# Optimization experiments

Hardware: AMD Instinct MI355X
Metric: run time of the kernel (lower is better)

The kernel has to match this reference:

```python
import jax, jax.numpy as jnp
import numpy as np

B, T = 64, 256
IN, HID, OUT = 512, 1024, 256
NUM_DOMAINS = 20

def setup_inputs() -> dict:
    key = jax.random.key(0)
    k1, k2, k3, k4 = jax.random.split(key, 4)
    x = jax.random.normal(k1, (B, T, IN), dtype=jnp.float32)
    hetero_info = jax.random.randint(k2, (B, 2), 0, NUM_DOMAINS, dtype=jnp.int64)
    # embedding tables init N(0, 0.02) as in the torch module
    fc1_table = 0.02 * jax.random.normal(k3, (NUM_DOMAINS, IN * HID + HID), dtype=jnp.float32)
    fc2_table = 0.02 * jax.random.normal(k4, (NUM_DOMAINS, HID * OUT + OUT), dtype=jnp.float32)
    return {"x": x, "hetero_info": hetero_info, "fc1_table": fc1_table, "fc2_table": fc2_table}

def reference(x, hetero_info, fc1_table, fc2_table):
    domain_id = hetero_info[:, 0].astype(jnp.int32)
    Bn = domain_id.shape[0]
    fc1_param = fc1_table[domain_id]                     # (B, IN*HID + HID)
    w1 = fc1_param[:, : IN * HID].reshape(Bn, IN, HID)   # (B, IN, HID)
    b1 = fc1_param[:, IN * HID:].reshape(Bn, 1, HID)
    fc2_param = fc2_table[domain_id]                     # (B, HID*OUT + OUT)
    w2 = fc2_param[:, : HID * OUT].reshape(Bn, HID, OUT) # (B, HID, OUT)
    b2 = fc2_param[:, HID * OUT:].reshape(Bn, 1, OUT)
    h = jnp.einsum('bti,bih->bth', x, w1) + b1
    h = jax.nn.gelu(h, approximate=False)  # torch nn.GELU default = exact erf
    out = jnp.einsum('bth,bho->bto', h, w2) + b2
    return out
```

## Files before the change

### kernel.cpp

```cpp
#include <hip/hip_runtime.h>
#include <math.h>

#define B_  64
#define T_  256
#define IN_ 512
#define HID_ 1024
#define OUT_ 256
#define NDOM 20

typedef __bf16 bf16_t;
typedef __bf16 bf16x8 __attribute__((ext_vector_type(8)));
typedef __bf16 bf16x4 __attribute__((ext_vector_type(4)));
typedef float  f32x4  __attribute__((ext_vector_type(4)));

__device__ __forceinline__ unsigned f2bf_bits(float f) {
    unsigned u = __builtin_bit_cast(unsigned, f);
    return (u + 0x7FFFu + ((u >> 16) & 1u)) >> 16;
}
__device__ __forceinline__ unsigned pack_bf16x2(float x, float y) {
    return f2bf_bits(x) | (f2bf_bits(y) << 16);
}

__device__ __forceinline__ void gl_lds16(const void* g, void* l) {
    __builtin_amdgcn_global_load_lds(
        (const __attribute__((address_space(1))) unsigned*)g,
        (__attribute__((address_space(3))) unsigned*)l,
        16, 0, 0);
}

__device__ __forceinline__ float gelu_fast(float v) {
    const float t = v * 0.70710678118654752f;
    const float a = __builtin_fabsf(t);
    const float k = __builtin_amdgcn_rcpf(__builtin_fmaf(0.3275911f, a, 1.0f));
    float p = __builtin_fmaf(1.061405429f, k, -1.453152027f);
    p = __builtin_fmaf(p, k, 1.421413741f);
    p = __builtin_fmaf(p, k, -0.284496736f);
    p = __builtin_fmaf(p, k, 0.254829592f);
    p = p * k;
    const float e  = __expf(-a * a);
    const float er = __builtin_fmaf(-p, e, 1.0f);
    const float erf_t = __builtin_copysignf(er, t);
    return 0.5f * v * (1.0f + erf_t);
}

template<int K, int N>
__global__ __launch_bounds__(256) void cvt_transpose(
    const float* __restrict__ table, bf16_t* __restrict__ Wt, float* __restrict__ BiasOut)
{
    const int d  = blockIdx.z;
    const float* W = table + (size_t)d * ((size_t)K * N + N);
    const int n0 = blockIdx.x * 64;
    const int k0 = blockIdx.y * 64;
    const int tid = threadIdx.x;

    __shared__ float t[64][65];

    #pragma unroll
    for (int r = 0; r < 4; ++r) {
        const int kl = (tid >> 4) + r * 16;
        const int nl = (tid & 15) * 4;
        float4 v = *(const float4*)(W + (size_t)(k0 + kl) * N + n0 + nl);
        t[kl][nl + 0] = v.x; t[kl][nl + 1] = v.y;
        t[kl][nl + 2] = v.z; t[kl][nl + 3] = v.w;
    }
    __syncthreads();

    bf16_t* Wtd = Wt + (size_t)d * K * N;
    #pragma unroll
    for (int r = 0; r < 4; ++r) {
        const int nl = (tid >> 4) + r * 16;
        const int k4 = (tid & 15) * 4;
        uint2 p;
        p.x = pack_bf16x2(t[k4 + 0][nl], t[k4 + 1][nl]);
        p.y = pack_bf16x2(t[k4 + 2][nl], t[k4 + 3][nl]);
        *(uint2*)(Wtd + (size_t)(n0 + nl) * K + k0 + k4) = p;
    }

    if (blockIdx.y == 0 && tid < 64)
        BiasOut[(size_t)d * N + n0 + tid] = W[(size_t)K * N + n0 + tid];
}

#define CT_STRIDE 136
__global__ __launch_bounds__(256) void fc1_gemm(
    const float*  __restrict__ X,
    const bf16_t* __restrict__ W1t,
    const float*  __restrict__ Bias,
    const int*    __restrict__ hetero,
    bf16_t*       __restrict__ H)
{
    const int id   = blockIdx.x;
    const int g    = id & 127;
    const int nidx = id >> 7;
    const int b    = g >> 1;
    const int m0   = (g & 1) * 128;
    const int n0   = nidx * 128;
    const int d    = hetero[2 * b];
    const bf16_t* W    = W1t + (size_t)d * HID_ * IN_;
    const float*  bias = Bias + (size_t)d * HID_;
    const float*  A    = X + (size_t)(b * 256 + m0) * IN_;

    __shared__ __attribute__((aligned(16))) char smem[65536];

    const int tid  = threadIdx.x;
    const int wave = tid >> 6;
    const int lane = tid & 63;
    const int l16  = lane & 15;
    const int quad = lane >> 4;
    const int wm   = (wave >> 1) * 64;
    const int wn   = (wave & 1) * 64;

    const int arow0 = tid >> 4;
    const int acol4 = tid & 15;

    f32x4 acc[4][4] = {};
    float4 pre[8];

    auto ldsA = [&](int nb) -> bf16_t* { return (bf16_t*)(smem + nb * 16384); };
    auto ldsB = [&](int nb) -> bf16_t* { return (bf16_t*)(smem + 32768 + nb * 16384); };

    auto loadA = [&](int kk) {
        #pragma unroll
        for (int r = 0; r < 8; ++r)
            pre[r] = *(const float4*)(A + (size_t)(arow0 + r * 16) * IN_ + kk + acol4 * 4);
    };
    auto writeA = [&](bf16_t* dst) {
        #pragma unroll
        for (int r = 0; r < 8; ++r) {
            const int row = arow0 + r * 16;
            const int cs  = (acol4 >> 1) ^ (row & 7);
            bf16x4 w;
            w[0] = (bf16_t)pre[r].x; w[1] = (bf16_t)pre[r].y;
            w[2] = (bf16_t)pre[r].z; w[3] = (bf16_t)pre[r].w;
            *(bf16x4*)&dst[row * 64 + cs * 8 + (acol4 & 1) * 4] = w;
        }
    };
    auto stageB = [&](int kk, bf16_t* dst) {
        #pragma unroll
        for (int cc = 0; cc < 4; ++cc) {
            const int r0  = wave * 32 + cc * 8;
            const int row = r0 + (lane >> 3);
            const int cs  = (lane & 7) ^ (row & 7);
            gl_lds16(W + (size_t)(n0 + row) * IN_ + kk + cs * 8, dst + r0 * 64);
        }
    };
    auto compute = [&](const bf16_t* La, const bf16_t* Lb) {
        #pragma unroll
        for (int h = 0; h < 2; ++h) {
            bf16x8 af[4], bfg[4];
            #pragma unroll
            for (int i = 0; i < 4; ++i) {
                const int r = wm + i * 16 + l16;
                const int c = (h * 4 + quad) ^ (r & 7);
                af[i] = *(const bf16x8*)&La[r * 64 + c * 8];
            }
            #pragma unroll
            for (int j = 0; j < 4; ++j) {
                const int r = wn + j * 16 + l16;
                const int c = (h * 4 + quad) ^ (r & 7);
                bfg[j] = *(const bf16x8*)&Lb[r * 64 + c * 8];
            }
            #pragma unroll
            for (int i = 0; i < 4; ++i)
                #pragma unroll
                for (int j = 0; j < 4; ++j)
                    acc[i][j] = __builtin_amdgcn_mfma_f32_16x16x32_bf16(bfg[j], af[i], acc[i][j], 0, 0, 0);
        }
    };

    loadA(0);
    stageB(0, ldsB(0));
    writeA(ldsA(0));
    __syncthreads();

    int buf = 0;
    for (int s = 0; s < 7; ++s) {
        loadA((s + 1) * 64);
        stageB((s + 1) * 64, ldsB(buf ^ 1));
        compute(ldsA(buf), ldsB(buf));
        writeA(ldsA(buf ^ 1));
        __syncthreads();
        buf ^= 1;
    }
    compute(ldsA(buf), ldsB(buf));
    __syncthreads();

    bf16_t* Ct = (bf16_t*)smem;

    #pragma unroll
    for (int i = 0; i < 4; ++i) {
        const int m = wm + i * 16 + l16;
        #pragma unroll
        for (int j = 0; j < 4; ++j) {
            const int nl = wn + j * 16 + quad * 4;
            const float4 b4 = *(const float4*)&bias[n0 + nl];
            bf16x4 w;
            w[0] = (bf16_t)gelu_fast(acc[i][j][0] + b4.x);
            w[1] = (bf16_t)gelu_fast(acc[i][j][1] + b4.y);
            w[2] = (bf16_t)gelu_fast(acc[i][j][2] + b4.z);
            w[3] = (bf16_t)gelu_fast(acc[i][j][3] + b4.w);
            *(bf16x4*)&Ct[m * CT_STRIDE + nl] = w;
        }
    }
    __syncthreads();

    #pragma unroll
    for (int it = 0; it < 8; ++it) {
        const int row = it * 16 + (tid >> 4);
        const int ch  = tid & 15;
        uint4 v = *(const uint4*)&Ct[row * CT_STRIDE + ch * 8];
        *(uint4*)&H[((size_t)(b * 256 + m0 + row)) * HID_ + n0 + ch * 8] = v;
    }
}

__global__ __launch_bounds__(256) void fc2_gemm(
    const bf16_t* __restrict__ H,
    const bf16_t* __restrict__ W2t,
    const float*  __restrict__ Bias,
    const int*    __restrict__ hetero,
    float*        __restrict__ Out)
{
    const int id   = blockIdx.x;
    const int g    = id & 255;
    const int nidx = id >> 8;
    const int b    = g >> 2;
    const int m0   = (g & 3) * 64;
    const int n0   = nidx * 64;
    const int d    = hetero[2 * b];
    const bf16_t* W    = W2t + (size_t)d * OUT_ * HID_;
    const float*  bias = Bias + (size_t)d * OUT_;

    __shared__ __attribute__((aligned(16))) bf16_t LdsA[2][64 * 64];
    __shared__ __attribute__((aligned(16))) bf16_t LdsB[2][64 * 64];

    const int tid  = threadIdx.x;
    const int wave = tid >> 6;
    const int lane = tid & 63;
    const int l16  = lane & 15;
    const int quad = lane >> 4;
    const int wm   = (wave >> 1) * 32;
    const int wn   = (wave & 1) * 32;

    f32x4 acc[2][2] = {};

    auto stage = [&](int kk, int nb) {
        #pragma unroll
        for (int cc = 0; cc < 2; ++cc) {
            const int r0  = wave * 16 + cc * 8;
            const int row = r0 + (lane >> 3);
            const int cs  = (lane & 7) ^ (row & 7);
            gl_lds16(H + (size_t)(b * 256 + m0 + row) * HID_ + kk + cs * 8,
                     &LdsA[nb][r0 * 64]);
            gl_lds16(W + (size_t)(n0 + row) * HID_ + kk + cs * 8,
                     &LdsB[nb][r0 * 64]);
        }
    };
    auto compute = [&](int nb) {
        #pragma unroll
        for (int h = 0; h < 2; ++h) {
            bf16x8 af[2], bfg[2];
            #pragma unroll
            for (int i = 0; i < 2; ++i) {
                const int r = wm + i * 16 + l16;
                const int c = (h * 4 + quad) ^ (r & 7);
                af[i] = *(const bf16x8*)&LdsA[nb][r * 64 + c * 8];
            }
            #pragma unroll
            for (int j = 0; j < 2; ++j) {
                const int r = wn + j * 16 + l16;
                const int c = (h * 4 + quad) ^ (r & 7);
                bfg[j] = *(const bf16x8*)&LdsB[nb][r * 64 + c * 8];
            }
            #pragma unroll
            for (int i = 0; i < 2; ++i)
                #pragma unroll
                for (int j = 0; j < 2; ++j)
                    acc[i][j] = __builtin_amdgcn_mfma_f32_16x16x32_bf16(bfg[j], af[i], acc[i][j], 0, 0, 0);
        }
    };

    stage(0, 0);
    __syncthreads();
    int buf = 0;
    for (int s = 0; s < 15; ++s) {
        stage((s + 1) * 64, buf ^ 1);
        compute(buf);
        __syncthreads();
        buf ^= 1;
    }
    compute(buf);

    #pragma unroll
    for (int i = 0; i < 2; ++i) {
        const int m = m0 + wm + i * 16 + l16;
        #pragma unroll
        for (int j = 0; j < 2; ++j) {
            const int nl = wn + j * 16 + quad * 4;
            const float4 b4 = *(const float4*)&bias[n0 + nl];
            float4 o;
            o.x = acc[i][j][0] + b4.x;
            o.y = acc[i][j][1] + b4.y;
            o.z = acc[i][j][2] + b4.z;
            o.w = acc[i][j][3] + b4.w;
            *(float4*)&Out[(size_t)(b * 256 + m) * OUT_ + n0 + nl] = o;
        }
    }
}

extern "C" void kernel_launch(void* const* d_in, const int* in_sizes, int n_in,
                              void* d_out, int out_size, void* d_ws, size_t ws_size,
                              hipStream_t stream) {
    const float* x         = (const float*)d_in[0];
    const int*   hetero    = (const int*)d_in[1];
    const float* fc1_table = (const float*)d_in[2];
    const float* fc2_table = (const float*)d_in[3];
    float*       out       = (float*)d_out;

    char* ws = (char*)d_ws;
    bf16_t* W1t = (bf16_t*)(ws);
    bf16_t* W2t = (bf16_t*)(ws + 20971520);
    float*  b1  = (float*)(ws + 31457280);
    float*  b2  = (float*)(ws + 31539200);
    bf16_t* H   = (bf16_t*)(ws + 31559680);

    cvt_transpose<IN_, HID_><<<dim3(HID_ / 64, IN_ / 64, NDOM), 256, 0, stream>>>(
        fc1_table, W1t, b1);
    cvt_transpose<HID_, OUT_><<<dim3(OUT_ / 64, HID_ / 64, NDOM), 256, 0, stream>>>(
        fc2_table, W2t, b2);

    fc1_gemm<<<dim3(1024), 256, 0, stream>>>(x, W1t, b1, hetero, H);
    fc2_gemm<<<dim3(1024), 256, 0, stream>>>(H, W2t, b2, hetero, out);
}
```

Measured before the change: 186.5 us.

## Pre-convert X to bf16, async-stage fc1 A tiles, widen fc2 N tile

Result: no change. 184.8 us (-0.9%).

```diff
diff --git a/kernel.cpp b/kernel.cpp
--- a/kernel.cpp
+++ b/kernel.cpp
@@ -43,6 +43,17 @@
     return 0.5f * v * (1.0f + erf_t);
 }
 
+__global__ __launch_bounds__(256) void cvt_x(
+    const float* __restrict__ X, bf16_t* __restrict__ Xbf)
+{
+    const size_t idx = (size_t)blockIdx.x * 256 + threadIdx.x;
+    float4 v = ((const float4*)X)[idx];
+    uint2 p;
+    p.x = pack_bf16x2(v.x, v.y);
+    p.y = pack_bf16x2(v.z, v.w);
+    ((uint2*)Xbf)[idx] = p;
+}
+
 template<int K, int N>
 __global__ __launch_bounds__(256) void cvt_transpose(
     const float* __restrict__ table, bf16_t* __restrict__ Wt, float* __restrict__ BiasOut)
@@ -82,7 +93,7 @@
 
 #define CT_STRIDE 136
 __global__ __launch_bounds__(256) void fc1_gemm(
-    const float*  __restrict__ X,
+    const bf16_t* __restrict__ Xbf,
     const bf16_t* __restrict__ W1t,
     const float*  __restrict__ Bias,
     const int*    __restrict__ hetero,
@@ -97,9 +108,9 @@
     const int d    = hetero[2 * b];
     const bf16_t* W    = W1t + (size_t)d * HID_ * IN_;
     const float*  bias = Bias + (size_t)d * HID_;
-    const float*  A    = X + (size_t)(b * 256 + m0) * IN_;
-
-    __shared__ __attribute__((aligned(16))) char smem[65536];
+    const bf16_t* A    = Xbf + (size_t)(b * 256 + m0) * IN_;
+
+    __shared__ __attribute__((aligned(16))) char smem[34816];
 
     const int tid  = threadIdx.x;
     const int wave = tid >> 6;
@@ -109,75 +120,59 @@
     const int wm   = (wave >> 1) * 64;
     const int wn   = (wave & 1) * 64;
 
-    const int arow0 = tid >> 4;
-    const int acol4 = tid & 15;
-
     f32x4 acc[4][4] = {};
-    float4 pre[8];
 
     auto ldsA = [&](int nb) -> bf16_t* { return (bf16_t*)(smem + nb * 16384); };
-    auto ldsB = [&](int nb) -> bf16_t* { return (bf16_t*)(smem + 32768 + nb * 16384); };
-
-    auto loadA = [&](int kk) {
-        #pragma unroll
-        for (int r = 0; r < 8; ++r)
-            pre[r] = *(const float4*)(A + (size_t)(arow0 + r * 16) * IN_ + kk + acol4 * 4);
-    };
-    auto writeA = [&](bf16_t* dst) {
-        #pragma unroll
-        for (int r = 0; r < 8; ++r) {
-            const int row = arow0 + r * 16;
-            const int cs  = (acol4 >> 1) ^ (row & 7);
-            bf16x4 w;
-            w[0] = (bf16_t)pre[r].x; w[1] = (bf16_t)pre[r].y;
-            w[2] = (bf16_t)pre[r].z; w[3] = (bf16_t)pre[r].w;
-            *(bf16x4*)&dst[row * 64 + cs * 8 + (acol4 & 1) * 4] = w;
+    auto ldsB = [&](int nb) -> bf16_t* { return (bf16_t*)(smem + 8192 + nb * 16384); };
+
+    auto stageA = [&](int kk, bf16_t* dst) {
+        #pragma unroll
+        for (int cc = 0; cc < 2; ++cc) {
+            const int r0  = wave * 32 + cc * 16;
+            const int row = r0 + (lane >> 2);
+            const int cs  = (lane & 3) ^ ((row >> 1) & 3);
+            gl_lds16(A + (size_t)row * IN_ + kk + cs * 8, dst + r0 * 32);
         }
     };
     auto stageB = [&](int kk, bf16_t* dst) {
         #pragma unroll
-        for (int cc = 0; cc < 4; ++cc) {
-            const int r0  = wave * 32 + cc * 8;
-            const int row = r0 + (lane >> 3);
-            const int cs  = (lane & 7) ^ (row & 7);
-            gl_lds16(W + (size_t)(n0 + row) * IN_ + kk + cs * 8, dst + r0 * 64);
+        for (int cc = 0; cc < 2; ++cc) {
+            const int r0  = wave * 32 + cc * 16;
+            const int row = r0 + (lane >> 2);
+            const int cs  = (lane & 3) ^ ((row >> 1) & 3);
+            gl_lds16(W + (size_t)(n0 + row) * IN_ + kk + cs * 8, dst + r0 * 32);
         }
     };
     auto compute = [&](const bf16_t* La, const bf16_t* Lb) {
-        #pragma unroll
-        for (int h = 0; h < 2; ++h) {
-            bf16x8 af[4], bfg[4];
+        bf16x8 af[4], bfg[4];
+        #pragma unroll
+        for (int i = 0; i < 4; ++i) {
+            const int r = wm + i * 16 + l16;
+            const int c = quad ^ ((r >> 1) & 3);
+            af[i] = *(const bf16x8*)&La[r * 32 + c * 8];
+        }
+        #pragma unroll
+        for (int j = 0; j < 4; ++j) {
+            const int r = wn + j * 16 + l16;
+            const int c = quad ^ ((r >> 1) & 3);
+            bfg[j] = *(const bf16x8*)&Lb[r * 32 + c * 8];
+        }
+        #pragma unroll
+        for (int i = 0; i < 4; ++i)
             #pragma unroll
-            for (int i = 0; i < 4; ++i) {
-                const int r = wm + i * 16 + l16;
-                const int c = (h * 4 + quad) ^ (r & 7);
-                af[i] = *(const bf16x8*)&La[r * 64 + c * 8];
-            }
-            #pragma unroll
-            for (int j = 0; j < 4; ++j) {
-                const int r = wn + j * 16 + l16;
-                const int c = (h * 4 + quad) ^ (r & 7);
-                bfg[j] = *(const bf16x8*)&Lb[r * 64 + c * 8];
-            }
-            #pragma unroll
-            for (int i = 0; i < 4; ++i)
-                #pragma unroll
-                for (int j = 0; j < 4; ++j)
-                    acc[i][j] = __builtin_amdgcn_mfma_f32_16x16x32_bf16(bfg[j], af[i], acc[i][j], 0, 0, 0);
-        }
-    };
-
-    loadA(0);
+            for (int j = 0; j < 4; ++j)
+                acc[i][j] = __builtin_amdgcn_mfma_f32_16x16x32_bf16(bfg[j], af[i], acc[i][j], 0, 0, 0);
+    };
+
+    stageA(0, ldsA(0));
     stageB(0, ldsB(0));
-    writeA(ldsA(0));
     __syncthreads();
 
     int buf = 0;
-    for (int s = 0; s < 7; ++s) {
-        loadA((s + 1) * 64);
-        stageB((s + 1) * 64, ldsB(buf ^ 1));
+    for (int s = 0; s < 15; ++s) {
+        stageA((s + 1) * 32, ldsA(buf ^ 1));
+        stageB((s + 1) * 32, ldsB(buf ^ 1));
         compute(ldsA(buf), ldsB(buf));
-        writeA(ldsA(buf ^ 1));
         __syncthreads();
         buf ^= 1;
     }
@@ -224,13 +219,13 @@
     const int nidx = id >> 8;
     const int b    = g >> 2;
     const int m0   = (g & 3) * 64;
-    const int n0   = nidx * 64;
+    const int n0   = nidx * 128;
     const int d    = hetero[2 * b];
     const bf16_t* W    = W2t + (size_t)d * OUT_ * HID_;
     const float*  bias = Bias + (size_t)d * OUT_;
-
-    __shared__ __attribute__((aligned(16))) bf16_t LdsA[2][64 * 64];
-    __shared__ __attribute__((aligned(16))) bf16_t LdsB[2][64 * 64];
+    const bf16_t* A    = H + (size_t)(b * 256 + m0) * HID_;
+
+    __shared__ __attribute__((aligned(16))) char smem[49152];
 
     const int tid  = threadIdx.x;
     const int wave = tid >> 6;
@@ -238,42 +233,53 @@
     const int l16  = lane & 15;
     const int quad = lane >> 4;
     const int wm   = (wave >> 1) * 32;
-    const int wn   = (wave & 1) * 32;
-
-    f32x4 acc[2][2] = {};
+    const int wn   = (wave & 1) * 64;
+
+    f32x4 acc[2][4] = {};
+
+    auto ldsA = [&](int nb) -> bf16_t* { return (bf16_t*)(smem + nb * 24576); };
+    auto ldsB = [&](int nb) -> bf16_t* { return (bf16_t*)(smem + 8192 + nb * 24576); };
 
     auto stage = [&](int kk, int nb) {
+        bf16_t* dA = ldsA(nb);
+        bf16_t* dB = ldsB(nb);
         #pragma unroll
         for (int cc = 0; cc < 2; ++cc) {
             const int r0  = wave * 16 + cc * 8;
             const int row = r0 + (lane >> 3);
             const int cs  = (lane & 7) ^ (row & 7);
-            gl_lds16(H + (size_t)(b * 256 + m0 + row) * HID_ + kk + cs * 8,
-                     &LdsA[nb][r0 * 64]);
-            gl_lds16(W + (size_t)(n0 + row) * HID_ + kk + cs * 8,
-                     &LdsB[nb][r0 * 64]);
+            gl_lds16(A + (size_t)row * HID_ + kk + cs * 8, dA + r0 * 64);
+        }
+        #pragma unroll
+        for (int cc = 0; cc < 4; ++cc) {
+            const int r0  = wave * 32 + cc * 8;
+            const int row = r0 + (lane >> 3);
+            const int cs  = (lane & 7) ^ (row & 7);
+            gl_lds16(W + (size_t)(n0 + row) * HID_ + kk + cs * 8, dB + r0 * 64);
         }
     };
     auto compute = [&](int nb) {
+        const bf16_t* La = ldsA(nb);
+        const bf16_t* Lb = ldsB(nb);
         #pragma unroll
         for (int h = 0; h < 2; ++h) {
-            bf16x8 af[2], bfg[2];
+            bf16x8 af[2], bfg[4];
             #pragma unroll
             for (int i = 0; i < 2; ++i) {
                 const int r = wm + i * 16 + l16;
                 const int c = (h * 4 + quad) ^ (r & 7);
-                af[i] = *(const bf16x8*)&LdsA[nb][r * 64 + c * 8];
+                af[i] = *(const bf16x8*)&La[r * 64 + c * 8];
             }
             #pragma unroll
-            for (int j = 0; j < 2; ++j) {
+            for (int j = 0; j < 4; ++j) {
                 const int r = wn + j * 16 + l16;
                 const int c = (h * 4 + quad) ^ (r & 7);
-                bfg[j] = *(const bf16x8*)&LdsB[nb][r * 64 + c * 8];
+                bfg[j] = *(const bf16x8*)&Lb[r * 64 + c * 8];
             }
             #pragma unroll
             for (int i = 0; i < 2; ++i)
                 #pragma unroll
-                for (int j = 0; j < 2; ++j)
+                for (int j = 0; j < 4; ++j)
                     acc[i][j] = __builtin_amdgcn_mfma_f32_16x16x32_bf16(bfg[j], af[i], acc[i][j], 0, 0, 0);
         }
     };
@@ -293,7 +299,7 @@
     for (int i = 0; i < 2; ++i) {
         const int m = m0 + wm + i * 16 + l16;
         #pragma unroll
-        for (int j = 0; j < 2; ++j) {
+        for (int j = 0; j < 4; ++j) {
             const int nl = wn + j * 16 + quad * 4;
             const float4 b4 = *(const float4*)&bias[n0 + nl];
             float4 o;
@@ -322,11 +328,14 @@
     float*  b2  = (float*)(ws + 31539200);
     bf16_t* H   = (bf16_t*)(ws + 31559680);
 
+    bf16_t* Xbf = (bf16_t*)d_out;
+
+    cvt_x<<<dim3(8192), 256, 0, stream>>>(x, Xbf);
     cvt_transpose<IN_, HID_><<<dim3(HID_ / 64, IN_ / 64, NDOM), 256, 0, stream>>>(
         fc1_table, W1t, b1);
     cvt_transpose<HID_, OUT_><<<dim3(OUT_ / 64, HID_ / 64, NDOM), 256, 0, stream>>>(
         fc2_table, W2t, b2);
 
-    fc1_gemm<<<dim3(1024), 256, 0, stream>>>(x, W1t, b1, hetero, H);
-    fc2_gemm<<<dim3(1024), 256, 0, stream>>>(H, W2t, b2, hetero, out);
-}
+    fc1_gemm<<<dim3(1024), 256, 0, stream>>>(Xbf, W1t, b1, hetero, H);
+    fc2_gemm<<<dim3(512), 256, 0, stream>>>(H, W2t, b2, hetero, out);
+}
```
